# Performance work log

Hardware: AMD Instinct MI355X
Metric: run time of the kernel (lower is better)

The kernel has to match this reference:

```python
import jax, jax.numpy as jnp
import numpy as np
import math

D_MODEL = 1024
NUM_HEADS = 16
D_K = D_MODEL // NUM_HEADS
ROPE_THETA = 10000.0


def _rope(x, pos):
    # x: [b, h, s, d], pos: [s] int -> apply interleaved rotary embedding
    d = x.shape[-1]
    inv_freq = 1.0 / (ROPE_THETA ** (jnp.arange(0, d, 2, dtype=jnp.float32) / d))  # [d/2]
    angles = pos.astype(jnp.float32)[:, None] * inv_freq  # [s, d/2]
    cos = jnp.cos(angles)  # broadcast to [1,1,s,d/2]
    sin = jnp.sin(angles)
    x1 = x[..., 0::2]
    x2 = x[..., 1::2]
    o1 = x1 * cos - x2 * sin
    o2 = x1 * sin + x2 * cos
    return jnp.stack([o1, o2], axis=-1).reshape(x.shape)


def setup_inputs() -> dict:
    key = jax.random.key(0)
    kx, kq, kk, kv, ko = jax.random.split(key, 5)
    scale = 1.0 / math.sqrt(D_MODEL)
    x = jax.random.normal(kx, (2, 2048, D_MODEL), dtype=jnp.float32)
    token_positions = jnp.arange(2048, dtype=jnp.int32)
    Wq = jax.random.normal(kq, (D_MODEL, D_MODEL), dtype=jnp.float32) * scale
    Wk = jax.random.normal(kk, (D_MODEL, D_MODEL), dtype=jnp.float32) * scale
    Wv = jax.random.normal(kv, (D_MODEL, D_MODEL), dtype=jnp.float32) * scale
    Wo = jax.random.normal(ko, (D_MODEL, D_MODEL), dtype=jnp.float32) * scale
    return {"x": x, "token_positions": token_positions, "Wq": Wq, "Wk": Wk, "Wv": Wv, "Wo": Wo}


def reference(x, token_positions, Wq, Wk, Wv, Wo):
    b, s, _ = x.shape
    h, dk = NUM_HEADS, D_K
    # Linear stores weight as [out, in]; y = x @ W.T
    def proj(W):
        y = jnp.einsum('bsm,nm->bsn', x, W)
        return y.reshape(b, s, h, dk).transpose(0, 2, 1, 3)  # [b,h,s,dk]
    Q = _rope(proj(Wq), token_positions)
    K = _rope(proj(Wk), token_positions)
    V = proj(Wv)
    scores = jnp.einsum('bhqd,bhkd->bhqk', Q, K) / math.sqrt(dk)
    causal = jnp.arange(s)[:, None] >= jnp.arange(s)[None, :]  # [s,s]
    scores = jnp.where(causal, scores, -jnp.inf)
    weights = jax.nn.softmax(scores, axis=-1)
    attn = jnp.einsum('bhqk,bhkd->bhqd', weights, V)  # [b,h,s,dk]
    attn = attn.transpose(0, 2, 1, 3).reshape(b, s, h * dk)
    return jnp.einsum('bsn,mn->bsm', attn, Wo)
```

## Files before the change

kernel.cpp:

```cpp
#include <hip/hip_runtime.h>
#include <math.h>

#define SEQ   2048
#define BATCH 2
#define NH    16
#define DKD   64
#define DM    1024
#define MTOT  (BATCH*SEQ)

typedef short bf16x8 __attribute__((ext_vector_type(8)));
typedef float f32x4  __attribute__((ext_vector_type(4)));
typedef unsigned short u16x4 __attribute__((ext_vector_type(4)));
typedef unsigned short u16x8 __attribute__((ext_vector_type(8)));

#define MFMA_B16(a,b,c) __builtin_amdgcn_mfma_f32_16x16x32_bf16((a),(b),(c),0,0,0)

__device__ __forceinline__ unsigned short f2bf(float f) {
    union { float f; unsigned int u; } v; v.f = f;
    unsigned int r = v.u + 0x7FFFu + ((v.u >> 16) & 1u);
    return (unsigned short)(r >> 16);
}
__device__ __forceinline__ float bf2f(unsigned short h) {
    union { unsigned int u; float f; } v; v.u = ((unsigned int)h) << 16;
    return v.f;
}
__device__ __forceinline__ void gload16(const void* g, void* l) {
    __builtin_amdgcn_global_load_lds(
        (const __attribute__((address_space(1))) unsigned int*)g,
        (__attribute__((address_space(3))) unsigned int*)l, 16, 0, 0);
}

__global__ __launch_bounds__(256)
void convert_all(const float* __restrict__ x,  const float* __restrict__ Wq,
                 const float* __restrict__ Wk, const float* __restrict__ Wv,
                 const float* __restrict__ Wo,
                 unsigned short* __restrict__ Xb, unsigned short* __restrict__ Wqkvb,
                 unsigned short* __restrict__ Wob)
{
    int i = blockIdx.x * 256 + threadIdx.x;
    const float* src;
    unsigned short* dst;
    size_t off;
    if (i < (1 << 19)) {
        src = x; dst = Xb; off = (size_t)i;
    } else {
        int j = i - (1 << 19);
        int wsel = j >> 17;
        off = (size_t)(j & ((1 << 17) - 1));
        src = (wsel == 0) ? Wq : (wsel == 1) ? Wk : (wsel == 2) ? Wv : Wo;
        dst = (wsel < 3) ? Wqkvb + (size_t)wsel * (1u << 20) : Wob;
    }
    float4 v0 = ((const float4*)src)[off * 2];
    float4 v1 = ((const float4*)src)[off * 2 + 1];
    u16x8 o = { f2bf(v0.x), f2bf(v0.y), f2bf(v0.z), f2bf(v0.w),
                f2bf(v1.x), f2bf(v1.y), f2bf(v1.z), f2bf(v1.w) };
    *(u16x8*)&dst[off * 8] = o;
}

__global__ __launch_bounds__(256)
void rope_bf16(unsigned short* __restrict__ Qb, unsigned short* __restrict__ Kb,
               const int* __restrict__ pos)
{
    int idx = blockIdx.x * 256 + threadIdx.x;
    int tsel = idx >> 19;
    int i = idx & ((1 << 19) - 1);
    unsigned short* base = tsel ? Kb : Qb;
    int d8 = i & 7;
    int s  = (i >> 3) & (SEQ - 1);
    float P = (float)pos[s];
    const float NEG_L2 = -0.41524101186092103f;

    u16x8 v = *(u16x8*)&base[(size_t)i * 8];
    u16x8 o;
    #pragma unroll
    for (int k = 0; k < 4; ++k) {
        int pi = d8 * 4 + k;
        float ang = P * exp2f((float)pi * NEG_L2);
        float sn, cs;
        sincosf(ang, &sn, &cs);
        float e0 = bf2f(v[2*k]), e1 = bf2f(v[2*k + 1]);
        o[2*k]     = f2bf(e0 * cs - e1 * sn);
        o[2*k + 1] = f2bf(e0 * sn + e1 * cs);
    }
    *(u16x8*)&base[(size_t)i * 8] = o;
}

template<int MODE>
__global__ __launch_bounds__(256)
void gemm_mfma(const unsigned short* __restrict__ A, const unsigned short* __restrict__ B,
               unsigned short* __restrict__ Qb, unsigned short* __restrict__ Kb,
               unsigned short* __restrict__ VTb, float* __restrict__ Cf)
{
    const int t = threadIdx.x;
    const int w = t >> 6, l = t & 63, lid = l & 15, hi = (l >> 4) * 16;
    const int wm = w >> 1, wn = w & 1;
    const int m0 = blockIdx.y * 128, n0 = blockIdx.x * 128;

    __shared__ __align__(16) char At[3][8192];
    __shared__ __align__(16) char Bt[3][8192];

    f32x4 acc[4][4];
    const f32x4 z4 = {0.f, 0.f, 0.f, 0.f};
    #pragma unroll
    for (int i = 0; i < 4; ++i)
        #pragma unroll
        for (int j = 0; j < 4; ++j) acc[i][j] = z4;

    const char* Ab = (const char*)A;
    const char* Bb = (const char*)B;

    auto stage = [&](int buf, int kt) {
        const int kbyte = kt * 64;
        #pragma unroll
        for (int i = 0; i < 2; ++i) {
            int o   = i * 4096 + t * 16;
            int row = o >> 6, cb = o & 63;
            int sw  = ((row >> 1) & 3) << 4;
            char* lbase_a = At[buf] + i * 4096 + (t >> 6) * 1024;
            char* lbase_b = Bt[buf] + i * 4096 + (t >> 6) * 1024;
            gload16(Ab + (size_t)(m0 + row) * 2048 + kbyte + (cb ^ sw), lbase_a);
            gload16(Bb + (size_t)(n0 + row) * 2048 + kbyte + (cb ^ sw), lbase_b);
        }
    };

    const int NKT = DM / 32;
    stage(0, 0);
    stage(1, 1);

    for (int kt = 0; kt < NKT; ++kt) {
        const int cur = kt % 3;
        if (kt == NKT - 1) asm volatile("s_waitcnt vmcnt(0)" ::: "memory");
        else               asm volatile("s_waitcnt vmcnt(4)" ::: "memory");
        __builtin_amdgcn_s_barrier();
        if (kt + 2 < NKT) stage((kt + 2) % 3, kt + 2);

        bf16x8 af[4], bfr[4];
        #pragma unroll
        for (int mf = 0; mf < 4; ++mf) {
            int ar = wm * 64 + mf * 16 + lid;
            af[mf] = *(const bf16x8*)(At[cur] + ar * 64 + (hi ^ (((ar >> 1) & 3) << 4)));
        }
        #pragma unroll
        for (int nf = 0; nf < 4; ++nf) {
            int br = wn * 64 + nf * 16 + lid;
            bfr[nf] = *(const bf16x8*)(Bt[cur] + br * 64 + (hi ^ (((br >> 1) & 3) << 4)));
        }
        __builtin_amdgcn_s_setprio(1);
        #pragma unroll
        for (int mf = 0; mf < 4; ++mf)
            #pragma unroll
            for (int nf = 0; nf < 4; ++nf)
                acc[mf][nf] = MFMA_B16(af[mf], bfr[nf], acc[mf][nf]);
        __builtin_amdgcn_s_setprio(0);
    }

    if (MODE == 1) {
        #pragma unroll
        for (int mf = 0; mf < 4; ++mf)
            #pragma unroll
            for (int nf = 0; nf < 4; ++nf) {
                int ncol = n0 + wn * 64 + nf * 16 + lid;
                #pragma unroll
                for (int jj = 0; jj < 4; ++jj) {
                    int mrow = m0 + wm * 64 + mf * 16 + (l >> 4) * 4 + jj;
                    Cf[(size_t)mrow * DM + ncol] = acc[mf][nf][jj];
                }
            }
    } else {
        const int z = n0 >> 10;
        const int nbase = n0 & 1023;
        #pragma unroll
        for (int mf = 0; mf < 4; ++mf)
            #pragma unroll
            for (int nf = 0; nf < 4; ++nf) {
                int ncol = nbase + wn * 64 + nf * 16 + lid;
                int h = ncol >> 6, d = ncol & 63;
                int mbase = m0 + wm * 64 + mf * 16 + (l >> 4) * 4;
                int b = mbase >> 11, s0v = mbase & 2047;
                if (z == 2) {
                    u16x4 pk = { f2bf(acc[mf][nf][0]), f2bf(acc[mf][nf][1]),
                                 f2bf(acc[mf][nf][2]), f2bf(acc[mf][nf][3]) };
                    *(u16x4*)&VTb[((size_t)(b * NH + h) * DKD + d) * SEQ + s0v] = pk;
                } else {
                    unsigned short* dst = (z == 0) ? Qb : Kb;
                    #pragma unroll
                    for (int jj = 0; jj < 4; ++jj)
                        dst[((size_t)(b * NH + h) * SEQ + (s0v + jj)) * DKD + d] =
                            f2bf(acc[mf][nf][jj]);
                }
            }
    }
}

__global__ __launch_bounds__(512)
void flash_mfma(const unsigned short* __restrict__ Qb, const unsigned short* __restrict__ Kb,
                const unsigned short* __restrict__ VTb, unsigned short* __restrict__ AOb)
{
    const int L  = blockIdx.y * 16 + blockIdx.x;
    const int g  = L >> 8, c = L & 255;
    const int j  = c & 15;
    const int bh = (g << 4) | (c >> 4);
    const int b = bh >> 4, h = bh & 15;
    const int qbA = g ? (30 - 2 * j) : (2 * j);
    const int qbB = qbA + 1;

    const int t = threadIdx.x;
    const int w8 = t >> 6, l = t & 63, lid = l & 15, hi = (l >> 4) * 16;
    const int h4 = l >> 4;
    const int tile = w8 >> 2, wq = w8 & 3;
    const int qbMy = tile ? qbB : qbA;
    const int ntMy = qbMy + 1;
    const int q0My = qbMy * 64;
    const int ntB  = qbB + 1;

    __shared__ __align__(16) char Kt[3][8192];
    __shared__ __align__(16) char Vt[3][8192];
    __shared__ __align__(16) char Pt[2][8192];

    const char* Kbh = (const char*)(Kb  + (size_t)bh * SEQ * DKD);
    const char* Vbh = (const char*)(VTb + (size_t)bh * SEQ * DKD);
    const char* Qbh = (const char*)(Qb  + (size_t)bh * SEQ * DKD);

    const f32x4 z4 = {0.f, 0.f, 0.f, 0.f};
    const int qrow = wq * 16 + lid;
    const float CLOG = 0.18033688011112042f;
    const float NMC  = -17.312340490667560f;

    bf16x8 onesv;
    #pragma unroll
    for (int i = 0; i < 8; ++i) onesv[i] = (short)0x3F80;

    bf16x8 qf[2];
    qf[0] = *(const bf16x8*)(Qbh + (size_t)(q0My + qrow) * 128 + 0  + hi);
    qf[1] = *(const bf16x8*)(Qbh + (size_t)(q0My + qrow) * 128 + 64 + hi);

    f32x4 o[4], o5;
    #pragma unroll
    for (int nf = 0; nf < 4; ++nf) o[nf] = z4;
    o5 = z4;

    auto stage = [&](int buf, int kt) {
        const int k0 = kt * 64;
        int o_  = t * 16;
        int row = o_ >> 7, cl = o_ & 127;
        int sw  = (row & 7) << 4;
        char* lK = Kt[buf] + w8 * 1024;
        char* lV = Vt[buf] + w8 * 1024;
        gload16(Kbh + (size_t)(k0 + row) * 128 + (cl ^ sw), lK);
        gload16(Vbh + (size_t)row * (SEQ * 2) + k0 * 2 + (cl ^ sw), lV);
    };

    stage(0, 0);
    stage(1, 1);

    for (int kt = 0; kt < ntB; ++kt) {
        const int cur = kt % 3;

        if (kt == ntB - 1) asm volatile("s_waitcnt vmcnt(0)" ::: "memory");
        else               asm volatile("s_waitcnt vmcnt(2)" ::: "memory");
        __builtin_amdgcn_s_barrier();
        if (kt + 2 < ntB) stage((kt + 2) % 3, kt + 2);

        if (kt < ntMy) {
            f32x4 sf[4];
            __builtin_amdgcn_s_setprio(1);
            #pragma unroll
            for (int nf = 0; nf < 4; ++nf) {
                f32x4 a = z4;
                #pragma unroll
                for (int ks = 0; ks < 2; ++ks) {
                    int r  = nf * 16 + lid;
                    int cb = ks * 64 + hi;
                    bf16x8 kfr = *(const bf16x8*)(Kt[cur] + r * 128 + (cb ^ ((r & 7) << 4)));
                    a = MFMA_B16(kfr, qf[ks], a);
                }
                sf[nf] = a;
            }
            __builtin_amdgcn_s_setprio(0);

            if (kt == qbMy) {
                const int qloc = wq * 16 + lid;
                #pragma unroll
                for (int nf = 0; nf < 4; ++nf) {
                    #pragma unroll
                    for (int jj = 0; jj < 4; ++jj) {
                        int keyloc = nf * 16 + h4 * 4 + jj;
                        if (keyloc > qloc) sf[nf][jj] = -1e30f;
                    }
                }
            }

            uint2 pk[4];
            #pragma unroll
            for (int nf = 0; nf < 4; ++nf) {
                float p0, p1, p2, p3;
                asm("v_exp_f32 %0, %1" : "=v"(p0) : "v"(fmaf(sf[nf][0], CLOG, NMC)));
                asm("v_exp_f32 %0, %1" : "=v"(p1) : "v"(fmaf(sf[nf][1], CLOG, NMC)));
                asm("v_exp_f32 %0, %1" : "=v"(p2) : "v"(fmaf(sf[nf][2], CLOG, NMC)));
                asm("v_exp_f32 %0, %1" : "=v"(p3) : "v"(fmaf(sf[nf][3], CLOG, NMC)));
                unsigned plo, phi;
                asm("v_cvt_pk_bf16_f32 %0, %1, %2" : "=v"(plo) : "v"(p0), "v"(p1));
                asm("v_cvt_pk_bf16_f32 %0, %1, %2" : "=v"(phi) : "v"(p2), "v"(p3));
                pk[nf].x = plo; pk[nf].y = phi;
            }

            {
                const int rowq = wq * 16 + lid;
                const int swz  = (lid & 7) << 4;
                char* base = Pt[tile] + rowq * 128;
                #pragma unroll
                for (int nf = 0; nf < 4; ++nf)
                    *(uint2*)(base + ((nf * 32 + 8 * h4) ^ swz)) = pk[nf];
            }

            #pragma unroll
            for (int ks = 0; ks < 2; ++ks) {
                int cb = ks * 64 + hi;
                int qr = wq * 16 + lid;
                bf16x8 pa = *(const bf16x8*)(Pt[tile] + qr * 128 + (cb ^ ((qr & 7) << 4)));
                __builtin_amdgcn_s_setprio(1);
                #pragma unroll
                for (int nf = 0; nf < 4; ++nf) {
                    int dr = nf * 16 + lid;
                    bf16x8 vb = *(const bf16x8*)(Vt[cur] + dr * 128 + (cb ^ ((dr & 7) << 4)));
                    o[nf] = MFMA_B16(pa, vb, o[nf]);
                }
                o5 = MFMA_B16(pa, onesv, o5);
                __builtin_amdgcn_s_setprio(0);
            }
        }
    }

    float inv[4];
    #pragma unroll
    for (int jj = 0; jj < 4; ++jj) inv[jj] = 1.0f / o5[jj];
    #pragma unroll
    for (int nf = 0; nf < 4; ++nf)
        #pragma unroll
        for (int jj = 0; jj < 4; ++jj) {
            int srow = q0My + wq * 16 + h4 * 4 + jj;
            int col  = h * 64 + nf * 16 + lid;
            AOb[((size_t)b * SEQ + srow) * DM + col] = f2bf(o[nf][jj] * inv[jj]);
        }
}

extern "C" void kernel_launch(void* const* d_in, const int* in_sizes, int n_in,
                              void* d_out, int out_size, void* d_ws, size_t ws_size,
                              hipStream_t stream)
{
    const float* x   = (const float*)d_in[0];
    const int*   pos = (const int*)  d_in[1];
    const float* Wq  = (const float*)d_in[2];
    const float* Wk  = (const float*)d_in[3];
    const float* Wv  = (const float*)d_in[4];
    const float* Wo  = (const float*)d_in[5];
    float* out = (float*)d_out;

    const size_t M1 = 1u << 20;
    unsigned short* ws  = (unsigned short*)d_ws;
    unsigned short* Xb    = ws;
    unsigned short* Wqkvb = ws + 4 * M1;
    unsigned short* Wob   = ws + 7 * M1;
    unsigned short* Qbf   = ws + 8 * M1;
    unsigned short* Kbf   = ws + 12 * M1;
    unsigned short* VTb   = ws + 16 * M1;
    unsigned short* AOb   = ws + 20 * M1;

    convert_all<<<4096, 256, 0, stream>>>(x, Wq, Wk, Wv, Wo, Xb, Wqkvb, Wob);

    gemm_mfma<0><<<dim3(24, 32), 256, 0, stream>>>(Xb, Wqkvb, Qbf, Kbf, VTb, nullptr);

    rope_bf16<<<4096, 256, 0, stream>>>(Qbf, Kbf, pos);

    flash_mfma<<<dim3(16, 32), 512, 0, stream>>>(Qbf, Kbf, VTb, AOb);

    gemm_mfma<1><<<dim3(8, 32), 256, 0, stream>>>(AOb, Wob, nullptr, nullptr, nullptr, out);
}
```

Baseline: 119.5 us.

## Software-pipeline QK and PV across iterations, pass P via shuffles

Restructures the attention loop so the QK^T scores for tile kt are computed while softmax and PV run on tile kt-1, with K staged three tiles ahead and V two tiles ahead in 4-deep LDS rings. The P tile is no longer written to and read back from shared memory; it is rebuilt into the MFMA A-operand layout with cross-lane shuffles. This aims to overlap MFMA work with exp/convert work and remove an LDS round-trip. In exchange it holds extra score registers, adds one more loop iteration, and uses more LDS for the deeper K/V rings.

```diff
diff --git a/kernel.cpp b/kernel.cpp
--- a/kernel.cpp
+++ b/kernel.cpp
@@ -213,9 +213,8 @@
     const int q0My = qbMy * 64;
     const int ntB  = qbB + 1;
 
-    __shared__ __align__(16) char Kt[3][8192];
-    __shared__ __align__(16) char Vt[3][8192];
-    __shared__ __align__(16) char Pt[2][8192];
+    __shared__ __align__(16) char Kt[4][8192];
+    __shared__ __align__(16) char Vt[4][8192];
 
     const char* Kbh = (const char*)(Kb  + (size_t)bh * SEQ * DKD);
     const char* Vbh = (const char*)(VTb + (size_t)bh * SEQ * DKD);
@@ -234,35 +233,40 @@
     qf[0] = *(const bf16x8*)(Qbh + (size_t)(q0My + qrow) * 128 + 0  + hi);
     qf[1] = *(const bf16x8*)(Qbh + (size_t)(q0My + qrow) * 128 + 64 + hi);
 
-    f32x4 o[4], o5;
-    #pragma unroll
-    for (int nf = 0; nf < 4; ++nf) o[nf] = z4;
+    f32x4 o[4], o5, sfP[4];
+    #pragma unroll
+    for (int nf = 0; nf < 4; ++nf) { o[nf] = z4; sfP[nf] = z4; }
     o5 = z4;
 
-    auto stage = [&](int buf, int kt) {
-        const int k0 = kt * 64;
-        int o_  = t * 16;
-        int row = o_ >> 7, cl = o_ & 127;
-        int sw  = (row & 7) << 4;
-        char* lK = Kt[buf] + w8 * 1024;
-        char* lV = Vt[buf] + w8 * 1024;
-        gload16(Kbh + (size_t)(k0 + row) * 128 + (cl ^ sw), lK);
-        gload16(Vbh + (size_t)row * (SEQ * 2) + k0 * 2 + (cl ^ sw), lV);
+    auto stageK = [&](int kt) {
+        int o_ = t * 16, row = o_ >> 7, cl = o_ & 127, sw = (row & 7) << 4;
+        gload16(Kbh + (size_t)(kt * 64 + row) * 128 + (cl ^ sw), Kt[kt & 3] + w8 * 1024);
     };
-
-    stage(0, 0);
-    stage(1, 1);
-
-    for (int kt = 0; kt < ntB; ++kt) {
-        const int cur = kt % 3;
-
-        if (kt == ntB - 1) asm volatile("s_waitcnt vmcnt(0)" ::: "memory");
-        else               asm volatile("s_waitcnt vmcnt(2)" ::: "memory");
+    auto stageV = [&](int kt) {
+        int o_ = t * 16, row = o_ >> 7, cl = o_ & 127, sw = (row & 7) << 4;
+        gload16(Vbh + (size_t)row * (SEQ * 2) + kt * 128 + (cl ^ sw), Vt[kt & 3] + w8 * 1024);
+    };
+
+    const int sl0 = lid + ((h4 & 1) << 5);
+    const int sl1 = sl0 + 16;
+    const bool selhi = (h4 >= 2);
+
+    stageK(0);
+    stageK(1);
+    stageV(0);
+    if (ntB >= 3) stageK(2);
+    stageV(1);
+
+    for (int kt = 0; kt <= ntB; ++kt) {
+        if (kt <= ntB - 4) asm volatile("s_waitcnt vmcnt(4)" ::: "memory");
+        else               asm volatile("s_waitcnt vmcnt(0)" ::: "memory");
         __builtin_amdgcn_s_barrier();
-        if (kt + 2 < ntB) stage((kt + 2) % 3, kt + 2);
-
-        if (kt < ntMy) {
-            f32x4 sf[4];
+        if (kt + 3 <= ntB - 1) stageK(kt + 3);
+        if (kt + 2 <= ntB - 1) stageV(kt + 2);
+
+        f32x4 sfN[4];
+        const bool doQK = (kt < ntMy);
+        if (doQK) {
             __builtin_amdgcn_s_setprio(1);
             #pragma unroll
             for (int nf = 0; nf < 4; ++nf) {
@@ -271,63 +275,74 @@
                 for (int ks = 0; ks < 2; ++ks) {
                     int r  = nf * 16 + lid;
                     int cb = ks * 64 + hi;
-                    bf16x8 kfr = *(const bf16x8*)(Kt[cur] + r * 128 + (cb ^ ((r & 7) << 4)));
+                    bf16x8 kfr = *(const bf16x8*)(Kt[kt & 3] + r * 128 + (cb ^ ((r & 7) << 4)));
                     a = MFMA_B16(kfr, qf[ks], a);
                 }
-                sf[nf] = a;
+                sfN[nf] = a;
             }
             __builtin_amdgcn_s_setprio(0);
-
-            if (kt == qbMy) {
+        }
+
+        if (kt >= 1 && (kt - 1) < ntMy) {
+            const int ktS = kt - 1;
+
+            if (ktS == qbMy) {
                 const int qloc = wq * 16 + lid;
                 #pragma unroll
-                for (int nf = 0; nf < 4; ++nf) {
+                for (int nf = 0; nf < 4; ++nf)
                     #pragma unroll
                     for (int jj = 0; jj < 4; ++jj) {
                         int keyloc = nf * 16 + h4 * 4 + jj;
-                        if (keyloc > qloc) sf[nf][jj] = -1e30f;
+                        if (keyloc > qloc) sfP[nf][jj] = -1e30f;
                     }
-                }
             }
 
             uint2 pk[4];
             #pragma unroll
             for (int nf = 0; nf < 4; ++nf) {
                 float p0, p1, p2, p3;
-                asm("v_exp_f32 %0, %1" : "=v"(p0) : "v"(fmaf(sf[nf][0], CLOG, NMC)));
-                asm("v_exp_f32 %0, %1" : "=v"(p1) : "v"(fmaf(sf[nf][1], CLOG, NMC)));
-                asm("v_exp_f32 %0, %1" : "=v"(p2) : "v"(fmaf(sf[nf][2], CLOG, NMC)));
-                asm("v_exp_f32 %0, %1" : "=v"(p3) : "v"(fmaf(sf[nf][3], CLOG, NMC)));
+                asm("v_exp_f32 %0, %1" : "=v"(p0) : "v"(fmaf(sfP[nf][0], CLOG, NMC)));
+                asm("v_exp_f32 %0, %1" : "=v"(p1) : "v"(fmaf(sfP[nf][1], CLOG, NMC)));
+                asm("v_exp_f32 %0, %1" : "=v"(p2) : "v"(fmaf(sfP[nf][2], CLOG, NMC)));
+                asm("v_exp_f32 %0, %1" : "=v"(p3) : "v"(fmaf(sfP[nf][3], CLOG, NMC)));
                 unsigned plo, phi;
                 asm("v_cvt_pk_bf16_f32 %0, %1, %2" : "=v"(plo) : "v"(p0), "v"(p1));
                 asm("v_cvt_pk_bf16_f32 %0, %1, %2" : "=v"(phi) : "v"(p2), "v"(p3));
                 pk[nf].x = plo; pk[nf].y = phi;
             }
 
-            {
-                const int rowq = wq * 16 + lid;
-                const int swz  = (lid & 7) << 4;
-                char* base = Pt[tile] + rowq * 128;
-                #pragma unroll
-                for (int nf = 0; nf < 4; ++nf)
-                    *(uint2*)(base + ((nf * 32 + 8 * h4) ^ swz)) = pk[nf];
-            }
-
             #pragma unroll
             for (int ks = 0; ks < 2; ++ks) {
+                unsigned A0x = __shfl((int)pk[2*ks    ].x, sl0);
+                unsigned A0y = __shfl((int)pk[2*ks    ].y, sl0);
+                unsigned A1x = __shfl((int)pk[2*ks + 1].x, sl0);
+                unsigned A1y = __shfl((int)pk[2*ks + 1].y, sl0);
+                unsigned B0x = __shfl((int)pk[2*ks    ].x, sl1);
+                unsigned B0y = __shfl((int)pk[2*ks    ].y, sl1);
+                unsigned B1x = __shfl((int)pk[2*ks + 1].x, sl1);
+                unsigned B1y = __shfl((int)pk[2*ks + 1].y, sl1);
+                union { unsigned u[4]; bf16x8 v; } pa;
+                pa.u[0] = selhi ? A1x : A0x;
+                pa.u[1] = selhi ? A1y : A0y;
+                pa.u[2] = selhi ? B1x : B0x;
+                pa.u[3] = selhi ? B1y : B0y;
+
                 int cb = ks * 64 + hi;
-                int qr = wq * 16 + lid;
-                bf16x8 pa = *(const bf16x8*)(Pt[tile] + qr * 128 + (cb ^ ((qr & 7) << 4)));
                 __builtin_amdgcn_s_setprio(1);
                 #pragma unroll
                 for (int nf = 0; nf < 4; ++nf) {
                     int dr = nf * 16 + lid;
-                    bf16x8 vb = *(const bf16x8*)(Vt[cur] + dr * 128 + (cb ^ ((dr & 7) << 4)));
-                    o[nf] = MFMA_B16(pa, vb, o[nf]);
+                    bf16x8 vb = *(const bf16x8*)(Vt[ktS & 3] + dr * 128 + (cb ^ ((dr & 7) << 4)));
+                    o[nf] = MFMA_B16(pa.v, vb, o[nf]);
                 }
-                o5 = MFMA_B16(pa, onesv, o5);
+                o5 = MFMA_B16(pa.v, onesv, o5);
                 __builtin_amdgcn_s_setprio(0);
             }
+        }
+
+        if (doQK) {
+            #pragma unroll
+            for (int nf = 0; nf < 4; ++nf) sfP[nf] = sfN[nf];
         }
     }
 
```

Measured after the change: 129.5 us. +8.4%, slower.

## Split flash attention key tiles across wave pairs with 1024-thread blocks

Applied to the files above, without the earlier changes.

Doubles the flash attention block to 1024 threads so each query row is handled by two waves, each taking half of the 64 keys in a tile (kh). Each wave computes half the scores and exponentials, then its PV MFMAs over its key half, and the two partial O and row-sum accumulators are combined through shared memory at the end. Staging is split so one half of the threads loads K and the other half loads V, with the wait count adjusted to match. This aims to give more waves in flight and shorten the per-wave critical path, at the cost of an extra reduction, barriers, and higher register pressure under the 1024-thread launch bound.

```diff
diff --git a/kernel.cpp b/kernel.cpp
--- a/kernel.cpp
+++ b/kernel.cpp
@@ -192,7 +192,7 @@
     }
 }
 
-__global__ __launch_bounds__(512)
+__global__ __launch_bounds__(1024, 8)
 void flash_mfma(const unsigned short* __restrict__ Qb, const unsigned short* __restrict__ Kb,
                 const unsigned short* __restrict__ VTb, unsigned short* __restrict__ AOb)
 {
@@ -207,7 +207,7 @@
     const int t = threadIdx.x;
     const int w8 = t >> 6, l = t & 63, lid = l & 15, hi = (l >> 4) * 16;
     const int h4 = l >> 4;
-    const int tile = w8 >> 2, wq = w8 & 3;
+    const int tile = w8 >> 3, wq = (w8 >> 1) & 3, kh = w8 & 1;
     const int qbMy = tile ? qbB : qbA;
     const int ntMy = qbMy + 1;
     const int q0My = qbMy * 64;
@@ -240,14 +240,15 @@
     o5 = z4;
 
     auto stage = [&](int buf, int kt) {
-        const int k0 = kt * 64;
-        int o_  = t * 16;
-        int row = o_ >> 7, cl = o_ & 127;
-        int sw  = (row & 7) << 4;
-        char* lK = Kt[buf] + w8 * 1024;
-        char* lV = Vt[buf] + w8 * 1024;
-        gload16(Kbh + (size_t)(k0 + row) * 128 + (cl ^ sw), lK);
-        gload16(Vbh + (size_t)row * (SEQ * 2) + k0 * 2 + (cl ^ sw), lV);
+        if (t < 512) {
+            int o_ = t * 16, row = o_ >> 7, cl = o_ & 127, sw = (row & 7) << 4;
+            gload16(Kbh + (size_t)(kt * 64 + row) * 128 + (cl ^ sw),
+                    Kt[buf] + w8 * 1024);
+        } else {
+            int o_ = (t - 512) * 16, row = o_ >> 7, cl = o_ & 127, sw = (row & 7) << 4;
+            gload16(Vbh + (size_t)row * (SEQ * 2) + kt * 128 + (cl ^ sw),
+                    Vt[buf] + (w8 - 8) * 1024);
+        }
     };
 
     stage(0, 0);
@@ -257,19 +258,19 @@
         const int cur = kt % 3;
 
         if (kt == ntB - 1) asm volatile("s_waitcnt vmcnt(0)" ::: "memory");
-        else               asm volatile("s_waitcnt vmcnt(2)" ::: "memory");
+        else               asm volatile("s_waitcnt vmcnt(1)" ::: "memory");
         __builtin_amdgcn_s_barrier();
         if (kt + 2 < ntB) stage((kt + 2) % 3, kt + 2);
 
         if (kt < ntMy) {
-            f32x4 sf[4];
+            f32x4 sf[2];
             __builtin_amdgcn_s_setprio(1);
             #pragma unroll
-            for (int nf = 0; nf < 4; ++nf) {
+            for (int nf = 0; nf < 2; ++nf) {
                 f32x4 a = z4;
                 #pragma unroll
                 for (int ks = 0; ks < 2; ++ks) {
-                    int r  = nf * 16 + lid;
+                    int r  = kh * 32 + nf * 16 + lid;
                     int cb = ks * 64 + hi;
                     bf16x8 kfr = *(const bf16x8*)(Kt[cur] + r * 128 + (cb ^ ((r & 7) << 4)));
                     a = MFMA_B16(kfr, qf[ks], a);
@@ -281,18 +282,18 @@
             if (kt == qbMy) {
                 const int qloc = wq * 16 + lid;
                 #pragma unroll
-                for (int nf = 0; nf < 4; ++nf) {
+                for (int nf = 0; nf < 2; ++nf) {
                     #pragma unroll
                     for (int jj = 0; jj < 4; ++jj) {
-                        int keyloc = nf * 16 + h4 * 4 + jj;
+                        int keyloc = kh * 32 + nf * 16 + h4 * 4 + jj;
                         if (keyloc > qloc) sf[nf][jj] = -1e30f;
                     }
                 }
             }
 
-            uint2 pk[4];
-            #pragma unroll
-            for (int nf = 0; nf < 4; ++nf) {
+            uint2 pk[2];
+            #pragma unroll
+            for (int nf = 0; nf < 2; ++nf) {
                 float p0, p1, p2, p3;
                 asm("v_exp_f32 %0, %1" : "=v"(p0) : "v"(fmaf(sf[nf][0], CLOG, NMC)));
                 asm("v_exp_f32 %0, %1" : "=v"(p1) : "v"(fmaf(sf[nf][1], CLOG, NMC)));
@@ -305,19 +306,16 @@
             }
 
             {
-                const int rowq = wq * 16 + lid;
                 const int swz  = (lid & 7) << 4;
-                char* base = Pt[tile] + rowq * 128;
-                #pragma unroll
-                for (int nf = 0; nf < 4; ++nf)
-                    *(uint2*)(base + ((nf * 32 + 8 * h4) ^ swz)) = pk[nf];
-            }
-
-            #pragma unroll
-            for (int ks = 0; ks < 2; ++ks) {
-                int cb = ks * 64 + hi;
-                int qr = wq * 16 + lid;
-                bf16x8 pa = *(const bf16x8*)(Pt[tile] + qr * 128 + (cb ^ ((qr & 7) << 4)));
+                char* base = Pt[tile] + qrow * 128;
+                #pragma unroll
+                for (int nf = 0; nf < 2; ++nf)
+                    *(uint2*)(base + ((kh * 64 + nf * 32 + 8 * h4) ^ swz)) = pk[nf];
+            }
+
+            {
+                int cb = kh * 64 + hi;
+                bf16x8 pa = *(const bf16x8*)(Pt[tile] + qrow * 128 + (cb ^ ((qrow & 7) << 4)));
                 __builtin_amdgcn_s_setprio(1);
                 #pragma unroll
                 for (int nf = 0; nf < 4; ++nf) {
@@ -331,17 +329,38 @@
         }
     }
 
-    float inv[4];
-    #pragma unroll
-    for (int jj = 0; jj < 4; ++jj) inv[jj] = 1.0f / o5[jj];
-    #pragma unroll
-    for (int nf = 0; nf < 4; ++nf)
-        #pragma unroll
-        for (int jj = 0; jj < 4; ++jj) {
-            int srow = q0My + wq * 16 + h4 * 4 + jj;
-            int col  = h * 64 + nf * 16 + lid;
-            AOb[((size_t)b * SEQ + srow) * DM + col] = f2bf(o[nf][jj] * inv[jj]);
-        }
+    __syncthreads();
+    const int ww = w8 >> 1;
+    char* scr = (ww < 4) ? ((char*)Kt + ww * 5120)
+                         : ((char*)Vt + (ww - 4) * 5120);
+    if (kh == 1) {
+        #pragma unroll
+        for (int nf = 0; nf < 4; ++nf)
+            *(f32x4*)(scr + l * 80 + nf * 16) = o[nf];
+        *(f32x4*)(scr + l * 80 + 64) = o5;
+    }
+    __syncthreads();
+    if (kh == 0) {
+        #pragma unroll
+        for (int nf = 0; nf < 4; ++nf) {
+            f32x4 po = *(const f32x4*)(scr + l * 80 + nf * 16);
+            o[nf] += po;
+        }
+        f32x4 po5 = *(const f32x4*)(scr + l * 80 + 64);
+        o5 += po5;
+
+        float inv[4];
+        #pragma unroll
+        for (int jj = 0; jj < 4; ++jj) inv[jj] = 1.0f / o5[jj];
+        #pragma unroll
+        for (int nf = 0; nf < 4; ++nf)
+            #pragma unroll
+            for (int jj = 0; jj < 4; ++jj) {
+                int srow = q0My + wq * 16 + h4 * 4 + jj;
+                int col  = h * 64 + nf * 16 + lid;
+                AOb[((size_t)b * SEQ + srow) * DM + col] = f2bf(o[nf][jj] * inv[jj]);
+            }
+    }
 }
 
 extern "C" void kernel_launch(void* const* d_in, const int* in_sizes, int n_in,
@@ -372,7 +391,7 @@
 
     rope_bf16<<<4096, 256, 0, stream>>>(Qbf, Kbf, pos);
 
-    flash_mfma<<<dim3(16, 32), 512, 0, stream>>>(Qbf, Kbf, VTb, AOb);
+    flash_mfma<<<dim3(16, 32), 1024, 0, stream>>>(Qbf, Kbf, VTb, AOb);
 
     gemm_mfma<1><<<dim3(8, 32), 256, 0, stream>>>(AOb, Wob, nullptr, nullptr, nullptr, out);
 }
```

After: 114.0 us. 4.6% less time.
